# Kernel optimization log

Hardware: AMD Instinct MI355X
Metric: run time of the kernel (lower is better)

The kernel has to match this reference:

```python
import jax, jax.numpy as jnp
from jax import lax
import numpy as np

EPS = 1e-5
K = 16
NUM_GROUP = 128
D = 384
HEADS = 6
DEPTH = 4
BETA = 0.25

def gelu(x):
    return jax.nn.gelu(x, approximate=False)

def linear(x, w, b):
    return x @ w.T + b

def layer_norm(x, g, b):
    mu = x.mean(-1, keepdims=True)
    var = x.var(-1, keepdims=True)
    return (x - mu) / jnp.sqrt(var + EPS) * g + b

def group_norm(x, gamma, beta, groups):
    B, C = x.shape[0], x.shape[1]
    sp = x.shape[2:]
    xg = x.reshape((B, groups, C // groups) + sp)
    axes = tuple(range(2, xg.ndim))
    mu = xg.mean(axes, keepdims=True)
    var = xg.var(axes, keepdims=True)
    xg = (xg - mu) / jnp.sqrt(var + EPS)
    x = xg.reshape((B, C) + sp)
    shp = (1, C) + (1,) * len(sp)
    return x * gamma.reshape(shp) + beta.reshape(shp)

def knn_idx(q, kp, k):
    # q [B,Nq,3], kp [B,Nk,3] -> idx [B,Nq,k] of k nearest keys
    d = jnp.sum(q * q, -1)[:, :, None] - 2.0 * jnp.einsum('bqd,bkd->bqk', q, kp) + jnp.sum(kp * kp, -1)[:, None, :]
    _, idx = lax.top_k(-d, k)
    return idx

def graph_feature(coor_q, x_q, coor_k, x_k, k):
    # coor [B,3,N], x [B,C,N] -> [B,2C,Nq,k]
    idx = knn_idx(coor_q.transpose(0, 2, 1), coor_k.transpose(0, 2, 1), k)
    feat = jax.vmap(lambda a, i: a[:, i])(x_k, idx)  # [B,C,Nq,k]
    xq = x_q[:, :, :, None]
    return jnp.concatenate([feat - xq, jnp.broadcast_to(xq, feat.shape)], axis=1)

def fps_indices(xyz, m):
    # farthest point sampling, start at index 0 (matches pointnet2)
    B, N, _ = xyz.shape
    def body(carry, _):
        dist, far = carry
        c = jnp.take_along_axis(xyz, far[:, None, None], axis=1)
        d = jnp.sum((xyz - c) ** 2, -1)
        dist = jnp.minimum(dist, d)
        return (dist, jnp.argmax(dist, -1).astype(jnp.int32)), far
    init = (jnp.full((B, N), 1e10, xyz.dtype), jnp.zeros((B,), jnp.int32))
    _, idxs = lax.scan(body, init, None, length=m)
    return idxs.T  # [B,m]

def gather_ch(x, idx):
    return jax.vmap(lambda a, i: a[:, i])(x, idx)

def conv1x1_2d(x, w):
    return jnp.einsum('oc,bcnk->bonk', w, x)

def conv1x1_1d(x, w, b):
    return jnp.einsum('oc,bcn->bon', w, x) + b[None, :, None]

def linear_resize(x, out_len):
    # F.interpolate(mode='linear', align_corners=False) along axis 1 of [B,N,D]
    n = x.shape[1]
    pos = (jnp.arange(out_len, dtype=x.dtype) + 0.5) * (n / out_len) - 0.5
    pos = jnp.clip(pos, 0.0, n - 1.0)
    i0 = jnp.floor(pos).astype(jnp.int32)
    i1 = jnp.minimum(i0 + 1, n - 1)
    w = (pos - i0.astype(x.dtype))[None, :, None]
    return x[:, i0] * (1.0 - w) + x[:, i1] * w

def vq(z, cb, beta):
    d = jnp.sum(z * z, -1, keepdims=True) - 2.0 * (z @ cb.T) + jnp.sum(cb * cb, -1)
    eidx = jnp.argmin(d, -1)
    q = cb[eidx]
    loss = jnp.mean((lax.stop_gradient(z) - q) ** 2) + beta * jnp.mean((z - lax.stop_gradient(q)) ** 2)
    q_st = z + lax.stop_gradient(q - z)  # straight-through
    return q_st, loss, eidx

def forward_core(xyz, it_w, it_b, g1_w, g1_g, g1_bt, g2_w, g2_g, g2_bt, g3_w, g3_g, g3_bt, g4_w, g4_g, g4_bt, pe_w1, pe_b1, pe_w2, pe_b2, ip_w1, ip_b1, ip_w2, ip_b2, ln1_g, ln1_b, qkv_w, qkv_b, o_w, o_b, ln2_g, ln2_b, m1_w, m1_b, m2_w, m2_b, pyr_w1, pyr_b1, pyr_g1, pyr_bt1, pyr_w2, pyr_b2, pyr_g2, pyr_bt2, fus_w, fus_b, cb0, cb1, cb2):
    B = xyz.shape[0]
    x = xyz.transpose(0, 2, 1)  # [B,7,N]
    coor, normal, plane = x[:, :3], x[:, 3:6], x[:, 6:7]
    f = conv1x1_1d(coor, it_w, it_b)  # [B,8,N]

    def edge_conv(cq, fq, ck, fk, w, g, bt, groups):
        h = graph_feature(cq, fq, ck, fk, K)
        h = conv1x1_2d(h, w)
        h = group_norm(h, g, bt, groups)
        h = jnp.where(h > 0, h, 0.2 * h)  # LeakyReLU(0.2)
        return h.max(axis=-1)

    f = edge_conv(coor, f, coor, f, g1_w, g1_g, g1_bt, 4)  # [B,32,N]
    idx = fps_indices(coor.transpose(0, 2, 1), NUM_GROUP)
    coor_q, normal_q, plane_q, f_q = gather_ch(coor, idx), gather_ch(normal, idx), gather_ch(plane, idx), gather_ch(f, idx)
    f = edge_conv(coor_q, f_q, coor, f, g2_w, g2_g, g2_bt, 4)  # [B,64,128]
    coor, normal, plane = coor_q, normal_q, plane_q
    f = edge_conv(coor, f, coor, f, g3_w, g3_g, g3_bt, 4)  # [B,64,128]
    idx = fps_indices(coor.transpose(0, 2, 1), NUM_GROUP)
    coor_q, normal_q, plane_q, f_q = gather_ch(coor, idx), gather_ch(normal, idx), gather_ch(plane, idx), gather_ch(f, idx)
    f = edge_conv(coor_q, f_q, coor, f, g4_w, g4_g, g4_bt, 4)  # [B,128,128]
    coor = coor_q.transpose(0, 2, 1)  # [B,128,3]
    f = f.transpose(0, 2, 1)          # [B,128,128]

    pe = linear(gelu(linear(coor, pe_w1, pe_b1)), pe_w2, pe_b2)
    h = linear(gelu(linear(f, ip_w1, ip_b1)), ip_w2, ip_b2)
    t = h + pe
    hd = D // HEADS
    scale = 1.0 / np.sqrt(hd)
    N = t.shape[1]
    for l in range(DEPTH):
        hn = layer_norm(t, ln1_g[l], ln1_b[l])
        qkv = hn @ qkv_w[l] + qkv_b[l]
        q, k_, v = jnp.split(qkv, 3, axis=-1)
        q = q.reshape(B, N, HEADS, hd)
        k_ = k_.reshape(B, N, HEADS, hd)
        v = v.reshape(B, N, HEADS, hd)
        att = jax.nn.softmax(jnp.einsum('bqhd,bkhd->bhqk', q, k_) * scale, axis=-1)
        o = jnp.einsum('bhqk,bkhd->bqhd', att, v).reshape(B, N, D)
        t = t + o @ o_w[l] + o_b[l]
        hn = layer_norm(t, ln2_g[l], ln2_b[l])
        t = t + gelu(hn @ m1_w[l] + m1_b[l]) @ m2_w[l] + m2_b[l]

    base = t  # [B,128,384]
    cbs = (cb0, cb1, cb2)
    outs, losses, idxs = [], [], []
    prev = None
    for level in range(3):
        res = max(base.shape[1] // (2 ** level), 8)
        if res == base.shape[1]:
            lf = base
        else:
            # adaptive_avg_pool1d with evenly dividing bins == reshape-mean
            lf = base.reshape(B, res, base.shape[1] // res, D).mean(2)
        c = lf.transpose(0, 2, 1)
        c = gelu(group_norm(conv1x1_1d(c, pyr_w1[level], pyr_b1[level]), pyr_g1[level], pyr_bt1[level], 8))
        c = gelu(group_norm(conv1x1_1d(c, pyr_w2[level], pyr_b2[level]), pyr_g2[level], pyr_bt2[level], 8))
        proc = c.transpose(0, 2, 1)
        if level > 0:
            pu = prev if prev.shape[1] == res else linear_resize(prev, res)
            proc = gelu(linear(jnp.concatenate([proc, pu], axis=-1), fus_w[level - 1], fus_b[level - 1]))
        q_st, loss, eidx = vq(proc, cbs[level], BETA)
        outs.append(q_st)
        losses.append(loss)
        idxs.append(eidx)
        prev = q_st
    return outs, losses, idxs

def setup_inputs():
    key = jax.random.key(0)
    cnt = [0]
    def nrm(shape, s=0.02):
        cnt[0] += 1
        return jax.random.normal(jax.random.fold_in(key, cnt[0]), shape, jnp.float32) * s
    L = 4
    inp = {}
    inp['xyz'] = nrm((8, 4096, 7), 1.0)
    inp['it_w'] = nrm((8, 3), 0.3)
    inp['it_b'] = jnp.zeros((8,), jnp.float32)
    inp['g1_w'] = nrm((32, 16), 0.1); inp['g1_g'] = jnp.ones((32,)); inp['g1_bt'] = jnp.zeros((32,))
    inp['g2_w'] = nrm((64, 64), 0.1); inp['g2_g'] = jnp.ones((64,)); inp['g2_bt'] = jnp.zeros((64,))
    inp['g3_w'] = nrm((64, 128), 0.1); inp['g3_g'] = jnp.ones((64,)); inp['g3_bt'] = jnp.zeros((64,))
    inp['g4_w'] = nrm((128, 128), 0.1); inp['g4_g'] = jnp.ones((128,)); inp['g4_bt'] = jnp.zeros((128,))
    inp['pe_w1'] = nrm((128, 3), 0.3); inp['pe_b1'] = jnp.zeros((128,))
    inp['pe_w2'] = nrm((D, 128), 0.05); inp['pe_b2'] = jnp.zeros((D,))
    inp['ip_w1'] = nrm((512, 128), 0.05); inp['ip_b1'] = jnp.zeros((512,))
    inp['ip_w2'] = nrm((D, 512), 0.03); inp['ip_b2'] = jnp.zeros((D,))
    inp['ln1_g'] = jnp.ones((L, D)); inp['ln1_b'] = jnp.zeros((L, D))
    inp['qkv_w'] = nrm((L, D, 3 * D)); inp['qkv_b'] = jnp.zeros((L, 3 * D))
    inp['o_w'] = nrm((L, D, D)); inp['o_b'] = jnp.zeros((L, D))
    inp['ln2_g'] = jnp.ones((L, D)); inp['ln2_b'] = jnp.zeros((L, D))
    inp['m1_w'] = nrm((L, D, 4 * D)); inp['m1_b'] = jnp.zeros((L, 4 * D))
    inp['m2_w'] = nrm((L, 4 * D, D)); inp['m2_b'] = jnp.zeros((L, D))
    inp['pyr_w1'] = nrm((3, 2 * D, D), 0.03); inp['pyr_b1'] = jnp.zeros((3, 2 * D))
    inp['pyr_g1'] = jnp.ones((3, 2 * D)); inp['pyr_bt1'] = jnp.zeros((3, 2 * D))
    inp['pyr_w2'] = nrm((3, D, 2 * D), 0.03); inp['pyr_b2'] = jnp.zeros((3, D))
    inp['pyr_g2'] = jnp.ones((3, D)); inp['pyr_bt2'] = jnp.zeros((3, D))
    inp['fus_w'] = nrm((2, D, 2 * D), 0.03); inp['fus_b'] = jnp.zeros((2, D))
    inp['cb0'] = nrm((8192, D), 0.5)
    inp['cb1'] = nrm((4096, D), 0.5)
    inp['cb2'] = nrm((2048, D), 0.5)
    return inp

def reference(xyz, it_w, it_b, g1_w, g1_g, g1_bt, g2_w, g2_g, g2_bt, g3_w, g3_g, g3_bt, g4_w, g4_g, g4_bt, pe_w1, pe_b1, pe_w2, pe_b2, ip_w1, ip_b1, ip_w2, ip_b2, ln1_g, ln1_b, qkv_w, qkv_b, o_w, o_b, ln2_g, ln2_b, m1_w, m1_b, m2_w, m2_b, pyr_w1, pyr_b1, pyr_g1, pyr_bt1, pyr_w2, pyr_b2, pyr_g2, pyr_bt2, fus_w, fus_b, cb0, cb1, cb2):
    outs, losses, idxs = forward_core(xyz, it_w, it_b, g1_w, g1_g, g1_bt, g2_w, g2_g, g2_bt, g3_w, g3_g, g3_bt, g4_w, g4_g, g4_bt, pe_w1, pe_b1, pe_w2, pe_b2, ip_w1, ip_b1, ip_w2, ip_b2, ln1_g, ln1_b, qkv_w, qkv_b, o_w, o_b, ln2_g, ln2_b, m1_w, m1_b, m2_w, m2_b, pyr_w1, pyr_b1, pyr_g1, pyr_bt1, pyr_w2, pyr_b2, pyr_g2, pyr_bt2, fus_w, fus_b, cb0, cb1, cb2)
    # concat quantized features of the 3 levels (128+64+32 tokens), total VQ loss, per-level indices
    return (jnp.concatenate(outs, axis=1), losses[0] + losses[1] + losses[2], idxs[0], idxs[1], idxs[2])
```

## Files before the change

kernel.cpp:

```cpp
#include <hip/hip_runtime.h>
#include <math.h>

#define EPSF 1e-5f

__device__ __forceinline__ float geluf(float x){
  return 0.5f*x*(1.0f + erff(x*0.70710678118654752440f));
}

typedef __attribute__((ext_vector_type(8))) short bf16x8;
typedef __attribute__((ext_vector_type(4))) float f32x4;

constexpr size_t WQKV = 0;
constexpr size_t WO   = WQKV + (size_t)4*1152*384;
constexpr size_t WM1  = WO   + (size_t)4*384*384;
constexpr size_t WM2  = WM1  + (size_t)4*1536*384;
constexpr size_t WIP1 = WM2  + (size_t)4*384*1536;
constexpr size_t WIP2 = WIP1 + (size_t)512*128;
constexpr size_t WPE2 = WIP2 + (size_t)384*512;
constexpr size_t WPY1 = WPE2 + (size_t)384*128;
constexpr size_t WPY2 = WPY1 + (size_t)3*768*384;
constexpr size_t WFUS = WPY2 + (size_t)3*384*768;
constexpr size_t WTOT = WFUS + (size_t)2*384*768;

__device__ __forceinline__ void split_rne(float x, short& h, short& l){
  union{float f; unsigned u;} xu; xu.f = x;
  unsigned lsb = (xu.u >> 16) & 1u;
  unsigned hb = (xu.u + 0x7fffu + lsb) >> 16;
  union{unsigned u; float f;} hf; hf.u = hb << 16;
  float lof = x - hf.f;
  union{float f; unsigned u;} lu; lu.f = lof;
  unsigned lsb2 = (lu.u >> 16) & 1u;
  unsigned lb = (lu.u + 0x7fffu + lsb2) >> 16;
  h = (short)hb;
  l = (short)lb;
}

__device__ __forceinline__ void split_quad(const float* src, unsigned* hi, unsigned* lo, size_t qdst){
  float4 v = *(const float4*)src;
  short h0,h1,h2,h3,l0,l1,l2,l3;
  split_rne(v.x,h0,l0); split_rne(v.y,h1,l1); split_rne(v.z,h2,l2); split_rne(v.w,h3,l3);
  hi[qdst*2+0] = ((unsigned)(unsigned short)h0) | (((unsigned)(unsigned short)h1)<<16);
  hi[qdst*2+1] = ((unsigned)(unsigned short)h2) | (((unsigned)(unsigned short)h3)<<16);
  lo[qdst*2+0] = ((unsigned)(unsigned short)l0) | (((unsigned)(unsigned short)l1)<<16);
  lo[qdst*2+1] = ((unsigned)(unsigned short)l2) | (((unsigned)(unsigned short)l3)<<16);
}


__global__ void init_pts(const float* __restrict__ xyz, const float* __restrict__ w,
                         const float* __restrict__ bias, float* __restrict__ coor,
                         float* __restrict__ f, int B, int N){
  int i = blockIdx.x*blockDim.x + threadIdx.x;
  if(i >= B*N) return;
  int n = i % N; int b = i / N;
  const float* p = xyz + (size_t)i*7;
  float x = p[0], y = p[1], z = p[2];
  coor[((size_t)b*3+0)*N+n] = x;
  coor[((size_t)b*3+1)*N+n] = y;
  coor[((size_t)b*3+2)*N+n] = z;
  float* fr = f + (size_t)i*8;
  #pragma unroll
  for(int c=0;c<8;c++)
    fr[c] = w[c*3+0]*x + w[c*3+1]*y + w[c*3+2]*z + bias[c];
}

__global__ void transpose_cn(const float* __restrict__ src, float* __restrict__ dst, int B, int C, int N){
  int i = blockIdx.x*blockDim.x + threadIdx.x;
  if(i >= B*C*N) return;
  int c = i % C; int n = (i/C)%N; int b = i/(C*N);
  dst[i] = src[((size_t)b*C + c)*N + n];
}

__global__ void gather_ch_kernel(const float* __restrict__ src, const int* __restrict__ idx,
                                 float* __restrict__ dst, int B, int C, int N, int M){
  int i = blockIdx.x*blockDim.x + threadIdx.x;
  if(i >= B*C*M) return;
  int m = i % M; int c = (i/M)%C; int b = i/(C*M);
  dst[i] = src[((size_t)b*C + c)*N + idx[b*M + m]];
}

__global__ void gather_rows(const float* __restrict__ src, const int* __restrict__ idx,
                            float* __restrict__ dst, int B, int C, int N, int M){
  int i = blockIdx.x*blockDim.x + threadIdx.x;
  if(i >= B*M*C) return;
  int c = i % C; int m = (i/C)%M; int b = i/(C*M);
  dst[i] = src[((size_t)b*N + idx[b*M+m])*C + c];
}

__global__ void split_planes(const float* __restrict__ src, short* __restrict__ hi,
                             short* __restrict__ lo, int n4){
  int i = blockIdx.x*blockDim.x + threadIdx.x;
  if(i >= n4) return;
  split_quad(src + (size_t)i*4, (unsigned*)hi, (unsigned*)lo, i);
}

__global__ void split_cb3(const float* __restrict__ c0, const float* __restrict__ c1,
                          const float* __restrict__ c2, short* __restrict__ hi, short* __restrict__ lo){
  constexpr int N1 = 8192*384/4, N2 = 4096*384/4, N3 = 2048*384/4;
  int i = blockIdx.x*blockDim.x + threadIdx.x;
  if(i >= N1+N2+N3) return;
  const float* src; size_t q;
  if(i < N1){ src = c0; q = i; }
  else if(i < N1+N2){ src = c1; q = i - N1; }
  else { src = c2; q = i - N1 - N2; }
  split_quad(src + q*4, (unsigned*)hi, (unsigned*)lo, (size_t)i);
}

__global__ void cbsq3(const float* __restrict__ c0, const float* __restrict__ c1,
                      const float* __restrict__ c2, float* __restrict__ out){
  int c = blockIdx.x*blockDim.x + threadIdx.x;
  if(c >= 14336) return;
  const float* p;
  if(c < 8192) p = c0 + (size_t)c*384;
  else if(c < 12288) p = c1 + (size_t)(c-8192)*384;
  else p = c2 + (size_t)(c-12288)*384;
  float s=0.f;
  for(int d=0;d<384;d++) s = fmaf(p[d],p[d],s);
  out[c] = s;
}

__global__ void split_multi(const float* __restrict__ ip1, const float* __restrict__ ip2,
                            const float* __restrict__ pe2, const float* __restrict__ py1,
                            const float* __restrict__ py2, const float* __restrict__ fus,
                            short* __restrict__ hi, short* __restrict__ lo){
  constexpr int N1 = 512*128/4, N2 = 384*512/4, N3 = 384*128/4;
  constexpr int N4 = 3*768*384/4, N5 = 3*384*768/4, N6 = 2*384*768/4;
  int i = blockIdx.x*blockDim.x + threadIdx.x;
  const float* src; size_t q, dq;
  if(i < N1){ src=ip1; q=i; dq=WIP1/4+q; }
  else if(i < N1+N2){ src=ip2; q=i-N1; dq=WIP2/4+q; }
  else if(i < N1+N2+N3){ src=pe2; q=i-N1-N2; dq=WPE2/4+q; }
  else if(i < N1+N2+N3+N4){ src=py1; q=i-N1-N2-N3; dq=WPY1/4+q; }
  else if(i < N1+N2+N3+N4+N5){ src=py2; q=i-N1-N2-N3-N4; dq=WPY2/4+q; }
  else if(i < N1+N2+N3+N4+N5+N6){ src=fus; q=i-N1-N2-N3-N4-N5; dq=WFUS/4+q; }
  else return;
  split_quad(src + q*4, (unsigned*)hi, (unsigned*)lo, dq);
}

__global__ __launch_bounds__(256) void transpose_split(const float* __restrict__ src,
    short* __restrict__ hi, short* __restrict__ lo, int K, int N,
    size_t sstride, size_t dstride){
  __shared__ float tile[32][33];
  int l = blockIdx.z;
  src += (size_t)l*sstride; hi += (size_t)l*dstride; lo += (size_t)l*dstride;
  int bn = blockIdx.x*32, bk = blockIdx.y*32;
  int tx = threadIdx.x & 31, ty = threadIdx.x >> 5;
  #pragma unroll
  for(int i=ty; i<32; i+=8){
    int k = bk+i, n = bn+tx;
    tile[i][tx] = (k<K && n<N) ? src[(size_t)k*N+n] : 0.f;
  }
  __syncthreads();
  #pragma unroll
  for(int i=ty; i<32; i+=8){
    int n = bn+i, k = bk+tx;
    if(n<N && k<K){
      short h,l2; split_rne(tile[tx][i], h, l2);
      hi[(size_t)n*K+k] = h; lo[(size_t)n*K+k] = l2;
    }
  }
}

#define KNN_K 16
#define KNN_SLOTS 48
template<int NKMAX, int NT>
__global__ __launch_bounds__(NT) void knn4q_kernel(const float* __restrict__ Q, const float* __restrict__ Kp,
                                                   int* __restrict__ idxout, int B, int Nq, int Nk){
  constexpr int NW = NT/64;
  __shared__ float4 sk[NKMAX];
  __shared__ float scd[NW][4][KNN_SLOTS];
  __shared__ int   sci[NW][4][KNN_SLOTS];
  __shared__ int   scnt[NW][4];
  int qb = blockIdx.x*(NW*4);
  int b = qb / Nq;
  const float* kb = Kp + (size_t)b*3*Nk;
  if(threadIdx.x < NW*4) ((int*)scnt)[threadIdx.x] = 0;
  for(int n=threadIdx.x; n<Nk; n+=NT){
    float x = kb[n], y = kb[Nk+n], z = kb[2*Nk+n];
    sk[n] = make_float4(x, y, z, fmaf(x,x, fmaf(y,y, z*z)));
  }
  __syncthreads();
  int wave = threadIdx.x >> 6;
  int lane = threadIdx.x & 63;
  int nq0 = qb + wave*4 - b*Nq;
  float qx[4], qy[4], qz[4];
  #pragma unroll
  for(int qq=0;qq<4;qq++){
    qx[qq] = -2.0f*Q[((size_t)b*3+0)*Nq + nq0+qq];
    qy[qq] = -2.0f*Q[((size_t)b*3+1)*Nq + nq0+qq];
    qz[qq] = -2.0f*Q[((size_t)b*3+2)*Nq + nq0+qq];
  }

  float mind[4] = {INFINITY, INFINITY, INFINITY, INFINITY};
  for(int n=lane; n<Nk; n+=64){
    float4 k4 = sk[n];
    #pragma unroll
    for(int qq=0;qq<4;qq++){
      float d = fmaf(qx[qq], k4.x, fmaf(qy[qq], k4.y, fmaf(qz[qq], k4.z, k4.w)));
      mind[qq] = fminf(mind[qq], d);
    }
  }
  {
    float v0=mind[0], v1=mind[1], v2=mind[2], v3=mind[3];
    #pragma unroll
    for(int k=2;k<=64;k<<=1){
      #pragma unroll
      for(int j=k>>1;j>=1;j>>=1){
        float o0 = __shfl_xor(v0, j, 64);
        float o1 = __shfl_xor(v1, j, 64);
        float o2 = __shfl_xor(v2, j, 64);
        float o3 = __shfl_xor(v3, j, 64);
        bool keepmin = ((lane & j)==0) == ((lane & k)==0);
        v0 = keepmin ? fminf(v0,o0) : fmaxf(v0,o0);
        v1 = keepmin ? fminf(v1,o1) : fmaxf(v1,o1);
        v2 = keepmin ? fminf(v2,o2) : fmaxf(v2,o2);
        v3 = keepmin ? fminf(v3,o3) : fmaxf(v3,o3);
      }
    }
    mind[0]=v0; mind[1]=v1; mind[2]=v2; mind[3]=v3;
  }
  float tau[4];
  #pragma unroll
  for(int qq=0;qq<4;qq++) tau[qq] = __shfl(mind[qq], 15, 64);

  for(int n=lane; n<Nk; n+=64){
    float4 k4 = sk[n];
    #pragma unroll
    for(int qq=0;qq<4;qq++){
      float d = fmaf(qx[qq], k4.x, fmaf(qy[qq], k4.y, fmaf(qz[qq], k4.z, k4.w)));
      if(d <= tau[qq]){
        int slot = atomicAdd(&scnt[wave][qq], 1);
        if(slot < KNN_SLOTS){ scd[wave][qq][slot] = d; sci[wave][qq][slot] = n; }
      }
    }
  }
  __syncthreads();

  #pragma unroll
  for(int qq=0; qq<4; qq++){
// ... 424 lines not shown
        bl[n] = *(bf16x8*)&sBlo[bcol][half*32 + g*8];
      }
      #pragma unroll
      for(int m=0;m<2;m++){
        #pragma unroll
        for(int n=0;n<2;n++){
          acc[m][n] = __builtin_amdgcn_mfma_f32_16x16x32_bf16(ah[m], bh[n], acc[m][n], 0, 0, 0);
          acc[m][n] = __builtin_amdgcn_mfma_f32_16x16x32_bf16(ah[m], bl[n], acc[m][n], 0, 0, 0);
          acc[m][n] = __builtin_amdgcn_mfma_f32_16x16x32_bf16(al[m], bh[n], acc[m][n], 0, 0, 0);
        }
      }
    }
    __syncthreads();
  }
  #pragma unroll
  for(int n=0;n<2;n++){
    int col = bn + wn*32 + n*16 + rr;
    float bb = bias ? bias[col] : 0.f;
    #pragma unroll
    for(int m=0;m<2;m++){
      #pragma unroll
      for(int r4=0;r4<4;r4++){
        int row = bm + wm*32 + m*16 + g*4 + r4;
        float v = acc[m][n][r4] + bb;
        if(act==1) v = geluf(v);
        size_t o = (size_t)row*N + col;
        if(addto) v += C[o];
        C[o] = v;
      }
    }
  }
}

__global__ __launch_bounds__(256) void gemm_mfma_ps(const float* __restrict__ A,
    const short* __restrict__ Bhi, const short* __restrict__ Blo,
    const float* __restrict__ bias, float* __restrict__ C,
    int M, int N, int K, int act, int addto,
    const float* __restrict__ lng, const float* __restrict__ lnb)
{
  __shared__ short sAhi[64][72];
  __shared__ short sAlo[64][72];
  __shared__ short sBhi[64][72];
  __shared__ short sBlo[64][72];
  int t = threadIdx.x;
  int lane = t & 63, wave = t >> 6;
  int wm = wave >> 1, wn = wave & 1;
  int g = lane >> 4, rr = lane & 15;
  int bm = blockIdx.y*64, bn = blockIdx.x*64;
  f32x4 acc[2][2];
  #pragma unroll
  for(int m=0;m<2;m++)
    #pragma unroll
    for(int n=0;n<2;n++)
      #pragma unroll
      for(int r=0;r<4;r++) acc[m][n][r] = 0.f;

  int ar_ = t >> 2, akq = (t & 3)*16;
  float lmu = 0.f, lrstd = 0.f;
  if(lng) ln_row_stats(A, bm + ar_, K, akq, lmu, lrstd);

  float areg[16];
  bf16x8 pbh[2], pbl[2];
  auto loadA = [&](int k0){
    const float* ap = A + (size_t)(bm + ar_)*K + k0 + akq;
    *(float4*)&areg[0]  = *(const float4*)(ap);
    *(float4*)&areg[4]  = *(const float4*)(ap+4);
    *(float4*)&areg[8]  = *(const float4*)(ap+8);
    *(float4*)&areg[12] = *(const float4*)(ap+12);
  };
  auto loadB = [&](int k0){
    const short* hp = Bhi + (size_t)(bn + ar_)*K + k0 + akq;
    const short* lp = Blo + (size_t)(bn + ar_)*K + k0 + akq;
    pbh[0] = *(const bf16x8*)hp; pbh[1] = *(const bf16x8*)(hp+8);
    pbl[0] = *(const bf16x8*)lp; pbl[1] = *(const bf16x8*)(lp+8);
  };
  auto stageA = [&](int k0){
    #pragma unroll
    for(int v8=0; v8<2; v8++){
      bf16x8 h, l;
      #pragma unroll
      for(int j=0;j<8;j++){
        float x = areg[v8*8+j];
        if(lng){
          int kk = k0 + akq + v8*8 + j;
          x = (x - lmu)*lrstd*lng[kk] + lnb[kk];
        }
        short th, tl;
        split_rne(x, th, tl);
        h[j] = th; l[j] = tl;
      }
      *(bf16x8*)&sAhi[ar_][akq + v8*8] = h;
      *(bf16x8*)&sAlo[ar_][akq + v8*8] = l;
    }
  };
  auto stageB = [&](){
    *(bf16x8*)&sBhi[ar_][akq]   = pbh[0];
    *(bf16x8*)&sBhi[ar_][akq+8] = pbh[1];
    *(bf16x8*)&sBlo[ar_][akq]   = pbl[0];
    *(bf16x8*)&sBlo[ar_][akq+8] = pbl[1];
  };

  loadA(0); loadB(0);
  int nk = K >> 6;
  for(int ki=0; ki<nk; ki++){
    stageA(ki*64); stageB();
    __syncthreads();
    if(ki+1 < nk){ loadA((ki+1)*64); loadB((ki+1)*64); }
    #pragma unroll
    for(int half=0; half<2; half++){
      bf16x8 ah[2], al[2], bh[2], bl[2];
      #pragma unroll
      for(int m=0;m<2;m++){
        int arow = wm*32 + m*16 + rr;
        ah[m] = *(bf16x8*)&sAhi[arow][half*32 + g*8];
        al[m] = *(bf16x8*)&sAlo[arow][half*32 + g*8];
      }
      #pragma unroll
      for(int n=0;n<2;n++){
        int bcol = wn*32 + n*16 + rr;
        bh[n] = *(bf16x8*)&sBhi[bcol][half*32 + g*8];
        bl[n] = *(bf16x8*)&sBlo[bcol][half*32 + g*8];
      }
      #pragma unroll
      for(int m=0;m<2;m++){
        #pragma unroll
        for(int n=0;n<2;n++){
          acc[m][n] = __builtin_amdgcn_mfma_f32_16x16x32_bf16(ah[m], bh[n], acc[m][n], 0, 0, 0);
          acc[m][n] = __builtin_amdgcn_mfma_f32_16x16x32_bf16(ah[m], bl[n], acc[m][n], 0, 0, 0);
          acc[m][n] = __builtin_amdgcn_mfma_f32_16x16x32_bf16(al[m], bh[n], acc[m][n], 0, 0, 0);
        }
      }
    }
    __syncthreads();
  }
  #pragma unroll
  for(int n=0;n<2;n++){
    int col = bn + wn*32 + n*16 + rr;
    float bb = bias ? bias[col] : 0.f;
    #pragma unroll
    for(int m=0;m<2;m++){
      #pragma unroll
      for(int r4=0;r4<4;r4++){
        int row = bm + wm*32 + m*16 + g*4 + r4;
        float v = acc[m][n][r4] + bb;
        if(act==1) v = geluf(v);
        size_t o = (size_t)row*N + col;
        if(addto) v += C[o];
        C[o] = v;
      }
    }
  }
}

__global__ __launch_bounds__(256) void gemm_vq(const short* __restrict__ Ahi, const short* __restrict__ Alo,
    const short* __restrict__ Bhi, const short* __restrict__ Blo,
    const float* __restrict__ cbsq, unsigned long long* __restrict__ keys, int M, int N, int K)
{
  __shared__ short sAhi[64][72];
  __shared__ short sAlo[64][72];
  __shared__ short sBhi[64][72];
  __shared__ short sBlo[64][72];
  int t = threadIdx.x;
  int lane = t & 63, wave = t >> 6;
  int wm = wave >> 1, wn = wave & 1;
  int g = lane >> 4, rr = lane & 15;
  int bm = blockIdx.y*64, bn = blockIdx.x*64;
  f32x4 acc[2][2];
  #pragma unroll
  for(int m=0;m<2;m++)
    #pragma unroll
    for(int n=0;n<2;n++)
      #pragma unroll
      for(int r=0;r<4;r++) acc[m][n][r] = 0.f;

  int ar_ = t >> 2, akq = (t & 3)*16;
  bf16x8 pah[2], pal[2], pbh[2], pbl[2];
  auto loadT = [&](int k0){
    const short* hp = Ahi + (size_t)(bm + ar_)*K + k0 + akq;
    const short* lp = Alo + (size_t)(bm + ar_)*K + k0 + akq;
    pah[0] = *(const bf16x8*)hp; pah[1] = *(const bf16x8*)(hp+8);
    pal[0] = *(const bf16x8*)lp; pal[1] = *(const bf16x8*)(lp+8);
    const short* hq = Bhi + (size_t)(bn + ar_)*K + k0 + akq;
    const short* lq = Blo + (size_t)(bn + ar_)*K + k0 + akq;
    pbh[0] = *(const bf16x8*)hq; pbh[1] = *(const bf16x8*)(hq+8);
    pbl[0] = *(const bf16x8*)lq; pbl[1] = *(const bf16x8*)(lq+8);
  };
  auto stageT = [&](){
    *(bf16x8*)&sAhi[ar_][akq]   = pah[0];
    *(bf16x8*)&sAhi[ar_][akq+8] = pah[1];
    *(bf16x8*)&sAlo[ar_][akq]   = pal[0];
    *(bf16x8*)&sAlo[ar_][akq+8] = pal[1];
    *(bf16x8*)&sBhi[ar_][akq]   = pbh[0];
    *(bf16x8*)&sBhi[ar_][akq+8] = pbh[1];
    *(bf16x8*)&sBlo[ar_][akq]   = pbl[0];
    *(bf16x8*)&sBlo[ar_][akq+8] = pbl[1];
  };

  loadT(0);
  int nk = K >> 6;
  for(int ki=0; ki<nk; ki++){
    stageT();
    __syncthreads();
    if(ki+1 < nk) loadT((ki+1)*64);
    #pragma unroll
    for(int half=0; half<2; half++){
      bf16x8 ah[2], al[2], bh[2], bl[2];
      #pragma unroll
      for(int m=0;m<2;m++){
        int arow = wm*32 + m*16 + rr;
        ah[m] = *(bf16x8*)&sAhi[arow][half*32 + g*8];
        al[m] = *(bf16x8*)&sAlo[arow][half*32 + g*8];
      }
      #pragma unroll
      for(int n=0;n<2;n++){
        int bcol = wn*32 + n*16 + rr;
        bh[n] = *(bf16x8*)&sBhi[bcol][half*32 + g*8];
        bl[n] = *(bf16x8*)&sBlo[bcol][half*32 + g*8];
      }
      #pragma unroll
      for(int m=0;m<2;m++){
        #pragma unroll
        for(int n=0;n<2;n++){
          acc[m][n] = __builtin_amdgcn_mfma_f32_16x16x32_bf16(ah[m], bh[n], acc[m][n], 0, 0, 0);
          acc[m][n] = __builtin_amdgcn_mfma_f32_16x16x32_bf16(ah[m], bl[n], acc[m][n], 0, 0, 0);
          acc[m][n] = __builtin_amdgcn_mfma_f32_16x16x32_bf16(al[m], bh[n], acc[m][n], 0, 0, 0);
        }
      }
    }
    __syncthreads();
  }
  #pragma unroll
  for(int m=0;m<2;m++){
    #pragma unroll
    for(int r4=0;r4<4;r4++){
      int row = bm + wm*32 + m*16 + g*4 + r4;
      unsigned long long kmin = 0xFFFFFFFFFFFFFFFFull;
      #pragma unroll
      for(int n=0;n<2;n++){
        int col = bn + wn*32 + n*16 + rr;
        float v = cbsq[col] - 2.0f*acc[m][n][r4];
        union{float f; unsigned u;} vb; vb.f = v;
        unsigned s = (unsigned)((int)vb.u >> 31);
        unsigned mapped = vb.u ^ (s | 0x80000000u);
        unsigned long long key = ((unsigned long long)mapped << 32) | (unsigned)col;
        kmin = key < kmin ? key : kmin;
      }
      #pragma unroll
      for(int msk=1; msk<16; msk<<=1){
        unsigned long long o = __shfl_xor(kmin, msk, 64);
        kmin = o < kmin ? o : kmin;
      }
      if(rr == 0) atomicMin(&keys[row], kmin);
    }
  }
}

__global__ __launch_bounds__(512) void attn_kernel(const float* __restrict__ qkv, float* __restrict__ out){
  int bh = blockIdx.x; int b = bh/6, h = bh%6;
  __shared__ float sk[128][64]; __shared__ float sv[128][64];
  const float* base = qkv + (size_t)b*128*1152;
  for(int i=threadIdx.x;i<128*64;i+=512){
    int n = i>>6, d = i&63;
    sk[n][d] = base[(size_t)n*1152 + 384 + h*64 + d];
    sv[n][d] = base[(size_t)n*1152 + 768 + h*64 + d];
  }
  __syncthreads();
  int wave = threadIdx.x >> 6;
  int lane = threadIdx.x & 63;
  int part = lane >> 4;
  int n = wave*16 + (lane & 15);
  int d0 = part*16;
  float q[16];
  #pragma unroll
  for(int d=0;d<16;d++) q[d] = base[(size_t)n*1152 + h*64 + d0 + d];
  float m = -INFINITY, Z = 0.f;
  float acc[16];
  #pragma unroll
  for(int d=0;d<16;d++) acc[d]=0.f;
  for(int j=0;j<128;j++){
    float sp = 0.f;
    #pragma unroll
    for(int d=0;d<16;d++) sp = fmaf(q[d], sk[j][d0 + d], sp);
    float s = sp + __shfl_xor(sp, 16, 64);
    s = s + __shfl_xor(s, 32, 64);
    s *= 0.125f;
    if(s > m){
      float sc = expf(m - s);
      Z *= sc;
      #pragma unroll
      for(int d=0;d<16;d++) acc[d] *= sc;
      m = s;
    }
    float e = expf(s - m);
    Z += e;
    #pragma unroll
    for(int d=0;d<16;d++) acc[d] = fmaf(e, sv[j][d0 + d], acc[d]);
  }
  float invZ = 1.0f/Z;
  float* outp = out + ((size_t)b*128 + n)*384 + h*64 + d0;
  #pragma unroll
  for(int d=0;d<16;d++) outp[d] = acc[d]*invZ;
}

__global__ __launch_bounds__(256) void gn_gelu_kernel(float* __restrict__ x, const float* __restrict__ gamma,
                                                      const float* __restrict__ beta, int res, int C, int Cg){
  int b = blockIdx.x / 8; int gr = blockIdx.x % 8;
  int total = res*Cg;
  float s=0.f, q=0.f;
  for(int i=threadIdx.x;i<total;i+=256){
    int n = i/Cg, c = gr*Cg + i%Cg;
    float v = x[((size_t)b*res+n)*C + c];
    s += v; q += v*v;
  }
  __shared__ float rs[256], rq[256];
  rs[threadIdx.x]=s; rq[threadIdx.x]=q; __syncthreads();
  for(int st=128;st>0;st>>=1){
    if(threadIdx.x<st){ rs[threadIdx.x]+=rs[threadIdx.x+st]; rq[threadIdx.x]+=rq[threadIdx.x+st]; }
    __syncthreads();
  }
  float mean = rs[0]/(float)total;
  float var = rq[0]/(float)total - mean*mean; var = fmaxf(var, 0.f);
  float rstd = 1.0f/sqrtf(var+EPSF);
  __syncthreads();
  for(int i=threadIdx.x;i<total;i+=256){
    int n = i/Cg, c = gr*Cg + i%Cg;
    size_t off = ((size_t)b*res+n)*C + c;
    float hn = (x[off]-mean)*rstd*gamma[c] + beta[c];
    x[off] = geluf(hn);
  }
}

__global__ void pool_kernel(const float* __restrict__ t, float* __restrict__ lf, int B, int res, int r){
  int i = blockIdx.x*blockDim.x + threadIdx.x;
  if(i >= B*res*384) return;
  int c = i%384; int n = (i/384)%res; int b = i/(384*res);
  const float* tp = t + ((size_t)b*(res*r) + n*r)*384 + c;
  float v;
  if(r==2) v = (tp[0] + tp[384])*0.5f;
  else     v = ((tp[0]+tp[384]) + (tp[2*384]+tp[3*384]))*0.25f;
  lf[i] = v;
}

__global__ void pu_cat_kernel(const float* __restrict__ proc, const float* __restrict__ outbuf,
                              float* __restrict__ cat, int B, int res, int prevoff){
  int i = blockIdx.x*blockDim.x + threadIdx.x;
  if(i >= B*res*768) return;
  int c = i%768; int n = (i/768)%res; int b = i/(768*res);
  float v;
  if(c < 384) v = proc[((size_t)b*res+n)*384 + c];
  else {
    int cc = c-384;
    const float* p0 = outbuf + ((size_t)b*224 + prevoff + 2*n)*384 + cc;
    v = p0[0]*0.5f + p0[384]*0.5f;
  }
  cat[i] = v;
}

__global__ __launch_bounds__(128) void vq_out_kernel(const float* __restrict__ z,
    const unsigned long long* __restrict__ keys,
    const float* __restrict__ cb, float* __restrict__ out, float* __restrict__ lossacc,
    int res, int rowoff, float* __restrict__ idxout){
  int row = blockIdx.x;
  int b = row/res, n = row%res;
  int e = (int)(unsigned)(keys[row] & 0xffffffffull);
  const float* zr = z + (size_t)row*384;
  const float* q = cb + (size_t)e*384;
  float* o = out + ((size_t)b*224 + rowoff + n)*384;
  float ls = 0.f;
  for(int d=threadIdx.x; d<384; d+=128){
    float zd = zr[d], qd = q[d];
    o[d] = zd + (qd - zd);
    float df = zd - qd;
    ls = fmaf(df,df,ls);
  }
  __shared__ float red[128];
  red[threadIdx.x]=ls; __syncthreads();
  for(int st=64;st>0;st>>=1){ if(threadIdx.x<st) red[threadIdx.x]+=red[threadIdx.x+st]; __syncthreads(); }
  if(threadIdx.x==0){
    atomicAdd(lossacc, red[0]);
    idxout[row] = (float)e;
  }
}

__global__ void loss_kernel(const float* __restrict__ lossacc, float* __restrict__ out){
  float m0 = lossacc[0]/(8.0f*128.0f*384.0f);
  float m1 = lossacc[1]/(8.0f*64.0f*384.0f);
  float m2 = lossacc[2]/(8.0f*32.0f*384.0f);
  out[0] = (m0 + 0.25f*m0) + (m1 + 0.25f*m1) + (m2 + 0.25f*m2);
}


extern "C" void kernel_launch(void* const* d_in, const int* in_sizes, int n_in,
// ... 36 lines not shown
  const float* m1_b  = (const float*)d_in[32];
  const float* m2_w  = (const float*)d_in[33];
  const float* m2_b  = (const float*)d_in[34];
  const float* pyr_w1 = (const float*)d_in[35];
  const float* pyr_b1 = (const float*)d_in[36];
  const float* pyr_g1 = (const float*)d_in[37];
  const float* pyr_bt1= (const float*)d_in[38];
  const float* pyr_w2 = (const float*)d_in[39];
  const float* pyr_b2 = (const float*)d_in[40];
  const float* pyr_g2 = (const float*)d_in[41];
  const float* pyr_bt2= (const float*)d_in[42];
  const float* fus_w  = (const float*)d_in[43];
  const float* fus_b  = (const float*)d_in[44];
  const float* cb0    = (const float*)d_in[45];
  const float* cb1    = (const float*)d_in[46];
  const float* cb2    = (const float*)d_in[47];

  float* ws  = (float*)d_ws;
  float* out = (float*)d_out;

  constexpr int B_ = 8, N0 = 4096, M0 = 128;
  constexpr size_t OFF_COOR0 = 0;
  constexpr size_t OFF_F0    = OFF_COOR0 + (size_t)B_*3*N0;
  constexpr size_t OFF_F1    = OFF_F0 + (size_t)B_*8*N0;
  constexpr size_t OFF_IDX1  = OFF_F1 + (size_t)B_*32*N0;
  constexpr size_t OFF_FPS1  = OFF_IDX1 + (size_t)B_*N0*16;
  constexpr size_t OFF_COOR1 = OFF_FPS1 + B_*M0;
  constexpr size_t OFF_F1Q   = OFF_COOR1 + B_*3*M0;
  constexpr size_t OFF_IDX2  = OFF_F1Q + B_*32*M0;
  constexpr size_t OFF_F2    = OFF_IDX2 + (size_t)B_*M0*16;
  constexpr size_t OFF_IDX3  = OFF_F2 + B_*64*M0;
  constexpr size_t OFF_F3    = OFF_IDX3 + (size_t)B_*M0*16;
  constexpr size_t OFF_FPS2  = OFF_F3 + B_*64*M0;
  constexpr size_t OFF_COOR2 = OFF_FPS2 + B_*M0;
  constexpr size_t OFF_F3Q   = OFF_COOR2 + B_*3*M0;
  constexpr size_t OFF_IDX4  = OFF_F3Q + B_*64*M0;
  constexpr size_t OFF_F4    = OFF_IDX4 + (size_t)B_*M0*16;
  constexpr size_t OFF_COORT = OFF_F4 + B_*128*M0;
  constexpr size_t OFF_TMP   = OFF_COORT + B_*M0*3;
  constexpr size_t OFF_T     = OFF_TMP + (size_t)1024*512;
  constexpr size_t OFF_QKV   = OFF_T + (size_t)1024*384;
  constexpr size_t OFF_ATT   = OFF_QKV + (size_t)1024*1152;
  constexpr size_t OFF_MID   = OFF_ATT + (size_t)1024*384;
  constexpr size_t OFF_LF    = OFF_MID + (size_t)1024*1536;
  constexpr size_t OFF_C1    = OFF_LF + (size_t)512*384;
  constexpr size_t OFF_C2    = OFF_C1 + (size_t)1024*768;
  constexpr size_t OFF_CAT   = OFF_C2 + (size_t)1024*384;
  constexpr size_t OFF_PROC  = OFF_CAT + (size_t)512*768;
  constexpr size_t OFF_KEYS  = OFF_PROC + (size_t)512*384;
  constexpr size_t OFF_LNMR  = OFF_KEYS + 3584;
  constexpr size_t OFF_CBSQ  = OFF_LNMR + 2048;
  constexpr size_t OFF_PART  = OFF_CBSQ + 14336;
  constexpr size_t OFF_MR    = OFF_PART + 32768;
  constexpr size_t OFF_LOSS  = OFF_MR + 64;
  constexpr size_t OFF_ZHI   = OFF_LOSS + 64;
  constexpr size_t OFF_ZLO   = OFF_ZHI + 196608;
  constexpr size_t OFF_CBHI  = OFF_ZLO + 196608;
  constexpr size_t OFF_CBLO  = OFF_CBHI + 2752512;
  constexpr size_t OFF_WHI = OFF_CBLO + 2752512;
  constexpr size_t OFF_WLO = OFF_WHI + (WTOT+1)/2;
  constexpr size_t OFF_END = OFF_WLO + (WTOT+1)/2;

  float* coor0 = ws + OFF_COOR0;
  float* f0    = ws + OFF_F0;
  float* f1    = ws + OFF_F1;
  int*   idx1  = (int*)(ws + OFF_IDX1);
  int*   fps1  = (int*)(ws + OFF_FPS1);
  float* coor1 = ws + OFF_COOR1;
  float* f1q   = ws + OFF_F1Q;
  int*   idx2  = (int*)(ws + OFF_IDX2);
  float* f2    = ws + OFF_F2;
  int*   idx3  = (int*)(ws + OFF_IDX3);
  float* f3    = ws + OFF_F3;
  int*   fps2  = (int*)(ws + OFF_FPS2);
  float* coor2 = ws + OFF_COOR2;
  float* f3q   = ws + OFF_F3Q;
  int*   idx4  = (int*)(ws + OFF_IDX4);
  float* f4    = ws + OFF_F4;
  float* coorT = ws + OFF_COORT;
  float* tmp   = ws + OFF_TMP;
  float* tbuf  = ws + OFF_T;
  float* qkvb  = ws + OFF_QKV;
  float* attb  = ws + OFF_ATT;
  float* midb  = ws + OFF_MID;
  float* lfb   = ws + OFF_LF;
  float* c1b   = ws + OFF_C1;
  float* c2b   = ws + OFF_C2;
  float* catb  = ws + OFF_CAT;
  float* procb = ws + OFF_PROC;
  unsigned long long* keys = (unsigned long long*)(ws + OFF_KEYS);
  float* cbsq  = ws + OFF_CBSQ;
  float* part  = ws + OFF_PART;
  float* mr    = ws + OFF_MR;
  float* lossa = ws + OFF_LOSS;
  short* zhi   = (short*)(ws + OFF_ZHI);
  short* zlo   = (short*)(ws + OFF_ZLO);
  short* cbhi  = (short*)(ws + OFF_CBHI);
  short* cblo  = (short*)(ws + OFF_CBLO);
  short* whi   = (short*)(ws + OFF_WHI);
  short* wlo   = (short*)(ws + OFF_WLO);

  bool presplit = ws_size >= OFF_END * sizeof(float);

  auto cdiv = [](int a, int b){ return (a+b-1)/b; };
  auto gemm_full = [&](const float* A, const float* Bm, const float* bias, float* C,
                       int M, int N, int K, int BT, int act, int addto,
                       const float* lng, const float* lnb){
    if(((K & 63) == 0) && ((N & 63) == 0) && ((M & 63) == 0)){
      dim3 g(N/64, M/64);
      gemm_mfma<<<g, 256, 0, stream>>>(A, Bm, bias, C, M, N, K, BT, act, addto, lng, lnb);
    } else {
      dim3 g(N/64, M/64), blk(128);
      gemm64<<<g, blk, 0, stream>>>(A, Bm, bias, C, M, N, K, BT, act, addto);
    }
  };
  auto gemmW = [&](const float* A, const float* W, size_t wofs, const float* bias, float* C,
                   int M, int N, int K, int BT, int act, int addto,
                   const float* lng, const float* lnb){
    if(presplit && ((K & 63) == 0) && ((N & 63) == 0) && ((M & 63) == 0)){
      dim3 g(N/64, M/64);
      gemm_mfma_ps<<<g, 256, 0, stream>>>(A, whi + wofs, wlo + wofs, bias, C, M, N, K, act, addto, lng, lnb);
    } else {
      gemm_full(A, W, bias, C, M, N, K, BT, act, addto, lng, lnb);
    }
  };

  hipMemsetAsync(lossa, 0, 8*sizeof(float), stream);
  hipMemsetAsync(keys, 0xFF, 1792*sizeof(unsigned long long), stream);

  init_pts<<<cdiv(B_*N0,256),256,0,stream>>>(xyz, it_w, it_b, coor0, f0, B_, N0);

  split_cb3<<<cdiv(14336*384/4,256),256,0,stream>>>(cb0, cb1, cb2, cbhi, cblo);
  cbsq3<<<cdiv(14336,256),256,0,stream>>>(cb0, cb1, cb2, cbsq);

  if(presplit){
    transpose_split<<<dim3(1152/32,384/32,4),256,0,stream>>>(qkv_w, whi+WQKV, wlo+WQKV, 384, 1152,
        (size_t)384*1152, (size_t)1152*384);
    transpose_split<<<dim3(384/32,384/32,4),256,0,stream>>>(o_w, whi+WO, wlo+WO, 384, 384,
        (size_t)384*384, (size_t)384*384);
    transpose_split<<<dim3(1536/32,384/32,4),256,0,stream>>>(m1_w, whi+WM1, wlo+WM1, 384, 1536,
        (size_t)384*1536, (size_t)1536*384);
    transpose_split<<<dim3(384/32,1536/32,4),256,0,stream>>>(m2_w, whi+WM2, wlo+WM2, 1536, 384,
        (size_t)1536*384, (size_t)384*1536);
    int totq = (512*128 + 384*512 + 384*128 + 3*768*384 + 3*384*768 + 2*384*768)/4;
    split_multi<<<cdiv(totq,256),256,0,stream>>>(ip_w1, ip_w2, pe_w2, pyr_w1, pyr_w2, fus_w, whi, wlo);
  }

  knn4q_kernel<4096,512><<<B_*N0/32,512,0,stream>>>(coor0, coor0, idx1, B_, N0, N0);
  ec_main<8,32><<<B_*32*N0/256,256,0,stream>>>(f0, f0, idx1, g1_w, f1, part, N0, N0);
  ec_reduce<<<32,256,0,stream>>>(part, mr, 32*N0/256, 1.0f/(8.0f*N0*16.0f));
  ec_norm<<<cdiv(B_*32*N0,256),256,0,stream>>>(f1, mr, g1_g, g1_bt, N0, 32, B_*32*N0);

  fps_kernel<4096,8,512><<<B_,512,0,stream>>>(coor0, fps1, N0, M0);
  gather_ch_kernel<<<cdiv(B_*3*M0,256),256,0,stream>>>(coor0, fps1, coor1, B_, 3, N0, M0);
  gather_rows<<<cdiv(B_*M0*32,256),256,0,stream>>>(f1, fps1, f1q, B_, 32, N0, M0);

  knn4q_kernel<4096,512><<<B_*M0/32,512,0,stream>>>(coor1, coor0, idx2, B_, M0, N0);
  ec_main<32,64><<<B_*64*M0/256,256,0,stream>>>(f1q, f1, idx2, g2_w, f2, part, M0, N0);
  ec_reduce<<<32,256,0,stream>>>(part, mr, 64*M0/256, 1.0f/(16.0f*M0*16.0f));
  ec_norm<<<cdiv(B_*64*M0,256),256,0,stream>>>(f2, mr, g2_g, g2_bt, M0, 64, B_*64*M0);

  knn4q_kernel<128,512><<<B_*M0/32,512,0,stream>>>(coor1, coor1, idx3, B_, M0, M0);
  ec_main<64,64><<<B_*64*M0/256,256,0,stream>>>(f2, f2, idx3, g3_w, f3, part, M0, M0);
  ec_reduce<<<32,256,0,stream>>>(part, mr, 64*M0/256, 1.0f/(16.0f*M0*16.0f));
  ec_norm<<<cdiv(B_*64*M0,256),256,0,stream>>>(f3, mr, g3_g, g3_bt, M0, 64, B_*64*M0);

  fps_kernel<128,1,128><<<B_,128,0,stream>>>(coor1, fps2, M0, M0);
  gather_ch_kernel<<<cdiv(B_*3*M0,256),256,0,stream>>>(coor1, fps2, coor2, B_, 3, M0, M0);
  gather_rows<<<cdiv(B_*M0*64,256),256,0,stream>>>(f3, fps2, f3q, B_, 64, M0, M0);

  knn4q_kernel<128,512><<<B_*M0/32,512,0,stream>>>(coor2, coor1, idx4, B_, M0, M0);
  ec_main<64,128><<<B_*128*M0/256,256,0,stream>>>(f3q, f3, idx4, g4_w, f4, part, M0, M0);
  ec_reduce<<<32,256,0,stream>>>(part, mr, 128*M0/256, 1.0f/(32.0f*M0*16.0f));
  ec_norm<<<cdiv(B_*128*M0,256),256,0,stream>>>(f4, mr, g4_g, g4_bt, M0, 128, B_*128*M0);

  transpose_cn<<<cdiv(B_*3*M0,256),256,0,stream>>>(coor2, coorT, B_, 3, M0);

  gemm_full(coorT, pe_w1, pe_b1, tmp, 1024, 128, 3, 1, 1, 0, nullptr, nullptr);
  gemmW(tmp, pe_w2, WPE2, pe_b2, tbuf, 1024, 384, 128, 1, 0, 0, nullptr, nullptr);
  gemmW(f4, ip_w1, WIP1, ip_b1, tmp, 1024, 512, 128, 1, 1, 0, nullptr, nullptr);
  gemmW(tmp, ip_w2, WIP2, ip_b2, tbuf, 1024, 384, 512, 1, 0, 1, nullptr, nullptr);

  for(int l=0;l<4;l++){
    gemmW(tbuf, qkv_w + (size_t)l*384*1152, WQKV + (size_t)l*1152*384, qkv_b + l*1152, qkvb,
          1024, 1152, 384, 0, 0, 0, ln1_g + l*384, ln1_b + l*384);
    attn_kernel<<<48,512,0,stream>>>(qkvb, attb);
    gemmW(attb, o_w + (size_t)l*384*384, WO + (size_t)l*384*384, o_b + l*384, tbuf,
          1024, 384, 384, 0, 0, 1, nullptr, nullptr);
    gemmW(tbuf, m1_w + (size_t)l*384*1536, WM1 + (size_t)l*1536*384, m1_b + l*1536, midb,
          1024, 1536, 384, 0, 1, 0, ln2_g + l*384, ln2_b + l*384);
    gemmW(midb, m2_w + (size_t)l*1536*384, WM2 + (size_t)l*384*1536, m2_b + l*384, tbuf,
          1024, 384, 1536, 0, 0, 1, nullptr, nullptr);
  }

  const float* cbs[3] = {cb0, cb1, cb2};
  const int ncodes[3] = {8192, 4096, 2048};
  const int cboff[3]  = {0, 8192, 12288};
  const int keyoff[3] = {0, 1024, 1536};
  const int rowoffs[3] = {0, 128, 192};
  const size_t OUT0 = (size_t)8*224*384;
  float* idxouts[3] = { out + OUT0 + 1, out + OUT0 + 1 + 1024, out + OUT0 + 1 + 1536 };

  for(int lv=0; lv<3; ++lv){
    int res = 128 >> lv;
    int rows = 8*res;
    const float* lf;
    if(lv==0){ lf = tbuf; }
    else {
      pool_kernel<<<cdiv(rows*384,256),256,0,stream>>>(tbuf, lfb, B_, res, 1<<lv);
      lf = lfb;
    }
    gemmW(lf, pyr_w1 + (size_t)lv*768*384, WPY1 + (size_t)lv*768*384, pyr_b1 + lv*768, c1b,
          rows, 768, 384, 1, 0, 0, nullptr, nullptr);
    gn_gelu_kernel<<<64,256,0,stream>>>(c1b, pyr_g1 + lv*768, pyr_bt1 + lv*768, res, 768, 96);
    gemmW(c1b, pyr_w2 + (size_t)lv*384*768, WPY2 + (size_t)lv*384*768, pyr_b2 + lv*384, c2b,
          rows, 384, 768, 1, 0, 0, nullptr, nullptr);
    gn_gelu_kernel<<<64,256,0,stream>>>(c2b, pyr_g2 + lv*384, pyr_bt2 + lv*384, res, 384, 48);
    const float* z = c2b;
    if(lv > 0){
      pu_cat_kernel<<<cdiv(rows*768,256),256,0,stream>>>(c2b, out, catb, B_, res, rowoffs[lv-1]);
      gemmW(catb, fus_w + (size_t)(lv-1)*384*768, WFUS + (size_t)(lv-1)*384*768, fus_b + (lv-1)*384, procb,
            rows, 384, 768, 1, 1, 0, nullptr, nullptr);
      z = procb;
    }
    split_planes<<<cdiv(rows*384/4,256),256,0,stream>>>(z, zhi, zlo, rows*384/4);
    gemm_vq<<<dim3(ncodes[lv]/64, rows/64), 256, 0, stream>>>(zhi, zlo,
        cbhi + (size_t)cboff[lv]*384, cblo + (size_t)cboff[lv]*384,
        cbsq + cboff[lv], keys + keyoff[lv], rows, ncodes[lv], 384);
    vq_out_kernel<<<rows,128,0,stream>>>(z, keys + keyoff[lv], cbs[lv], out, lossa + lv, res,
                                         rowoffs[lv], idxouts[lv]);
  }

  loss_kernel<<<1,1,0,stream>>>(lossa, out + OUT0);
}
```

Baseline: 1.474 ms.

## Enlarge VQ distance GEMM tile to 128x128 and fuse FPS gathers

The VQ nearest-code GEMM now uses 128x128 tiles instead of 64x64. Each wave computes a 64x64 sub-tile with a 4x4 grid of MFMA accumulators, which raises operand reuse from LDS and halves global loads per output. Separately, the coordinate gather and feature-row gather after each FPS step are merged into one launch to save kernel launches. The larger tile uses more LDS and more accumulator registers. It also produces far fewer blocks for the smaller pyramid levels, which may leave CUs idle.

After: 1.451 ms, median of 2. About the same (-1.5%).

```diff
diff --git a/kernel.cpp b/kernel.cpp
--- a/kernel.cpp
+++ b/kernel.cpp
@@ -70,20 +70,21 @@
   dst[i] = src[((size_t)b*C + c)*N + n];
 }
 
-__global__ void gather_ch_kernel(const float* __restrict__ src, const int* __restrict__ idx,
-                                 float* __restrict__ dst, int B, int C, int N, int M){
+__global__ void gather_both(const float* __restrict__ coor_src, const float* __restrict__ feat_src,
+                            const int* __restrict__ idx, float* __restrict__ coor_dst,
+                            float* __restrict__ feat_dst, int B, int C, int N, int M){
+  int total_c = B*3*M;
   int i = blockIdx.x*blockDim.x + threadIdx.x;
-  if(i >= B*C*M) return;
-  int m = i % M; int c = (i/M)%C; int b = i/(C*M);
-  dst[i] = src[((size_t)b*C + c)*N + idx[b*M + m]];
-}
-
-__global__ void gather_rows(const float* __restrict__ src, const int* __restrict__ idx,
-                            float* __restrict__ dst, int B, int C, int N, int M){
-  int i = blockIdx.x*blockDim.x + threadIdx.x;
-  if(i >= B*M*C) return;
-  int c = i % C; int m = (i/C)%M; int b = i/(C*M);
-  dst[i] = src[((size_t)b*N + idx[b*M+m])*C + c];
+  if(i < total_c){
+    int m = i % M; int c = (i/M)%3; int b = i/(3*M);
+    coor_dst[i] = coor_src[((size_t)b*3 + c)*N + idx[b*M + m]];
+  } else {
+    int j = i - total_c;
+    if(j < B*M*C){
+      int c = j % C; int m = (j/C)%M; int b = j/(C*M);
+      feat_dst[j] = feat_src[((size_t)b*N + idx[b*M+m])*C + c];
+    }
+  }
 }
 
 __global__ void split_planes(const float* __restrict__ src, short* __restrict__ hi,
@@ -814,48 +815,51 @@
   }
 }
 
-__global__ __launch_bounds__(256) void gemm_vq(const short* __restrict__ Ahi, const short* __restrict__ Alo,
+__global__ __launch_bounds__(256) void gemm_vq128(const short* __restrict__ Ahi, const short* __restrict__ Alo,
     const short* __restrict__ Bhi, const short* __restrict__ Blo,
     const float* __restrict__ cbsq, unsigned long long* __restrict__ keys, int M, int N, int K)
 {
-  __shared__ short sAhi[64][72];
-  __shared__ short sAlo[64][72];
-  __shared__ short sBhi[64][72];
-  __shared__ short sBlo[64][72];
+  __shared__ short sAhi[128][72];
+  __shared__ short sAlo[128][72];
+  __shared__ short sBhi[128][72];
+  __shared__ short sBlo[128][72];
   int t = threadIdx.x;
   int lane = t & 63, wave = t >> 6;
   int wm = wave >> 1, wn = wave & 1;
   int g = lane >> 4, rr = lane & 15;
-  int bm = blockIdx.y*64, bn = blockIdx.x*64;
-  f32x4 acc[2][2];
-  #pragma unroll
-  for(int m=0;m<2;m++)
-    #pragma unroll
-    for(int n=0;n<2;n++)
+  int bm = blockIdx.y*128, bn = blockIdx.x*128;
+  f32x4 acc[4][4];
+  #pragma unroll
+  for(int m=0;m<4;m++)
+    #pragma unroll
+    for(int n=0;n<4;n++)
       #pragma unroll
       for(int r=0;r<4;r++) acc[m][n][r] = 0.f;
 
-  int ar_ = t >> 2, akq = (t & 3)*16;
-  bf16x8 pah[2], pal[2], pbh[2], pbl[2];
+  int ar_ = t >> 1, akq = (t & 1)*32;
+  bf16x8 pah[4], pal[4], pbh[4], pbl[4];
   auto loadT = [&](int k0){
     const short* hp = Ahi + (size_t)(bm + ar_)*K + k0 + akq;
     const short* lp = Alo + (size_t)(bm + ar_)*K + k0 + akq;
-    pah[0] = *(const bf16x8*)hp; pah[1] = *(const bf16x8*)(hp+8);
-    pal[0] = *(const bf16x8*)lp; pal[1] = *(const bf16x8*)(lp+8);
+    pah[0] = *(const bf16x8*)hp;      pah[1] = *(const bf16x8*)(hp+8);
+    pah[2] = *(const bf16x8*)(hp+16); pah[3] = *(const bf16x8*)(hp+24);
+    pal[0] = *(const bf16x8*)lp;      pal[1] = *(const bf16x8*)(lp+8);
+    pal[2] = *(const bf16x8*)(lp+16); pal[3] = *(const bf16x8*)(lp+24);
     const short* hq = Bhi + (size_t)(bn + ar_)*K + k0 + akq;
     const short* lq = Blo + (size_t)(bn + ar_)*K + k0 + akq;
-    pbh[0] = *(const bf16x8*)hq; pbh[1] = *(const bf16x8*)(hq+8);
-    pbl[0] = *(const bf16x8*)lq; pbl[1] = *(const bf16x8*)(lq+8);
+    pbh[0] = *(const bf16x8*)hq;      pbh[1] = *(const bf16x8*)(hq+8);
+    pbh[2] = *(const bf16x8*)(hq+16); pbh[3] = *(const bf16x8*)(hq+24);
+    pbl[0] = *(const bf16x8*)lq;      pbl[1] = *(const bf16x8*)(lq+8);
+    pbl[2] = *(const bf16x8*)(lq+16); pbl[3] = *(const bf16x8*)(lq+24);
   };
   auto stageT = [&](){
-    *(bf16x8*)&sAhi[ar_][akq]   = pah[0];
-    *(bf16x8*)&sAhi[ar_][akq+8] = pah[1];
-    *(bf16x8*)&sAlo[ar_][akq]   = pal[0];
-    *(bf16x8*)&sAlo[ar_][akq+8] = pal[1];
-    *(bf16x8*)&sBhi[ar_][akq]   = pbh[0];
-    *(bf16x8*)&sBhi[ar_][akq+8] = pbh[1];
-    *(bf16x8*)&sBlo[ar_][akq]   = pbl[0];
-    *(bf16x8*)&sBlo[ar_][akq+8] = pbl[1];
+    #pragma unroll
+    for(int c=0;c<4;c++){
+      *(bf16x8*)&sAhi[ar_][akq + c*8] = pah[c];
+      *(bf16x8*)&sAlo[ar_][akq + c*8] = pal[c];
+      *(bf16x8*)&sBhi[ar_][akq + c*8] = pbh[c];
+      *(bf16x8*)&sBlo[ar_][akq + c*8] = pbl[c];
+    }
   };
 
   loadT(0);
@@ -866,23 +870,23 @@
     if(ki+1 < nk) loadT((ki+1)*64);
     #pragma unroll
     for(int half=0; half<2; half++){
-      bf16x8 ah[2], al[2], bh[2], bl[2];
-      #pragma unroll
-      for(int m=0;m<2;m++){
-        int arow = wm*32 + m*16 + rr;
+      bf16x8 ah[4], al[4], bh[4], bl[4];
+      #pragma unroll
+      for(int m=0;m<4;m++){
+        int arow = wm*64 + m*16 + rr;
         ah[m] = *(bf16x8*)&sAhi[arow][half*32 + g*8];
         al[m] = *(bf16x8*)&sAlo[arow][half*32 + g*8];
       }
       #pragma unroll
-      for(int n=0;n<2;n++){
-        int bcol = wn*32 + n*16 + rr;
+      for(int n=0;n<4;n++){
+        int bcol = wn*64 + n*16 + rr;
         bh[n] = *(bf16x8*)&sBhi[bcol][half*32 + g*8];
         bl[n] = *(bf16x8*)&sBlo[bcol][half*32 + g*8];
       }
       #pragma unroll
-      for(int m=0;m<2;m++){
+      for(int m=0;m<4;m++){
         #pragma unroll
-        for(int n=0;n<2;n++){
+        for(int n=0;n<4;n++){
           acc[m][n] = __builtin_amdgcn_mfma_f32_16x16x32_bf16(ah[m], bh[n], acc[m][n], 0, 0, 0);
           acc[m][n] = __builtin_amdgcn_mfma_f32_16x16x32_bf16(ah[m], bl[n], acc[m][n], 0, 0, 0);
           acc[m][n] = __builtin_amdgcn_mfma_f32_16x16x32_bf16(al[m], bh[n], acc[m][n], 0, 0, 0);
@@ -892,14 +896,14 @@
     __syncthreads();
   }
   #pragma unroll
-  for(int m=0;m<2;m++){
+  for(int m=0;m<4;m++){
     #pragma unroll
     for(int r4=0;r4<4;r4++){
-      int row = bm + wm*32 + m*16 + g*4 + r4;
+      int row = bm + wm*64 + m*16 + g*4 + r4;
       unsigned long long kmin = 0xFFFFFFFFFFFFFFFFull;
       #pragma unroll
-      for(int n=0;n<2;n++){
-        int col = bn + wn*32 + n*16 + rr;
+      for(int n=0;n<4;n++){
+        int col = bn + wn*64 + n*16 + rr;
         float v = cbsq[col] - 2.0f*acc[m][n][r4];
         union{float f; unsigned u;} vb; vb.f = v;
         unsigned s = (unsigned)((int)vb.u >> 31);
@@ -1242,8 +1246,7 @@
   ec_norm<<<cdiv(B_*32*N0,256),256,0,stream>>>(f1, mr, g1_g, g1_bt, N0, 32, B_*32*N0);
 
   fps_kernel<4096,8,512><<<B_,512,0,stream>>>(coor0, fps1, N0, M0);
-  gather_ch_kernel<<<cdiv(B_*3*M0,256),256,0,stream>>>(coor0, fps1, coor1, B_, 3, N0, M0);
-  gather_rows<<<cdiv(B_*M0*32,256),256,0,stream>>>(f1, fps1, f1q, B_, 32, N0, M0);
+  gather_both<<<cdiv(B_*3*M0 + B_*M0*32,256),256,0,stream>>>(coor0, f1, fps1, coor1, f1q, B_, 32, N0, M0);
 
   knn4q_kernel<4096,512><<<B_*M0/32,512,0,stream>>>(coor1, coor0, idx2, B_, M0, N0);
   ec_main<32,64><<<B_*64*M0/256,256,0,stream>>>(f1q, f1, idx2, g2_w, f2, part, M0, N0);
@@ -1256,8 +1259,7 @@
   ec_norm<<<cdiv(B_*64*M0,256),256,0,stream>>>(f3, mr, g3_g, g3_bt, M0, 64, B_*64*M0);
 
   fps_kernel<128,1,128><<<B_,128,0,stream>>>(coor1, fps2, M0, M0);
-  gather_ch_kernel<<<cdiv(B_*3*M0,256),256,0,stream>>>(coor1, fps2, coor2, B_, 3, M0, M0);
-  gather_rows<<<cdiv(B_*M0*64,256),256,0,stream>>>(f3, fps2, f3q, B_, 64, M0, M0);
+  gather_both<<<cdiv(B_*3*M0 + B_*M0*64,256),256,0,stream>>>(coor1, f3, fps2, coor2, f3q, B_, 64, M0, M0);
 
   knn4q_kernel<128,512><<<B_*M0/32,512,0,stream>>>(coor2, coor1, idx4, B_, M0, M0);
   ec_main<64,128><<<B_*128*M0/256,256,0,stream>>>(f3q, f3, idx4, g4_w, f4, part, M0, M0);
@@ -1314,7 +1316,7 @@
       z = procb;
     }
     split_planes<<<cdiv(rows*384/4,256),256,0,stream>>>(z, zhi, zlo, rows*384/4);
-    gemm_vq<<<dim3(ncodes[lv]/64, rows/64), 256, 0, stream>>>(zhi, zlo,
+    gemm_vq128<<<dim3(ncodes[lv]/128, rows/128), 256, 0, stream>>>(zhi, zlo,
         cbhi + (size_t)cboff[lv]*384, cblo + (size_t)cboff[lv]*384,
         cbsq + cboff[lv], keys + keyoff[lv], rows, ncodes[lv], 384);
     vq_out_kernel<<<rows,128,0,stream>>>(z, keys + keyoff[lv], cbs[lv], out, lossa + lv, res,
```
